# Kernel tuning notes

Measured on AMD Instinct MI355X. Metric: run time of the kernel, lower is better.

Reference implementation:

```python
import jax, jax.numpy as jnp
import numpy as np

N_NODES = 100000
NEG_SLOPE = 0.2


def gat_conv(x, edge_index, W, a_src, a_dst, bias):
    """PyG GATConv, heads=1, concat, add_self_loops=True."""
    N = x.shape[0]
    loop = jnp.arange(N, dtype=edge_index.dtype)
    src = jnp.concatenate([edge_index[0], loop])  # message sources j
    dst = jnp.concatenate([edge_index[1], loop])  # message targets i
    h = x @ W                                      # [N, out]
    asrc = h @ a_src                               # [N]
    adst = h @ a_dst                               # [N]
    e = jax.nn.leaky_relu(asrc[src] + adst[dst], NEG_SLOPE)   # [E+N]
    m = jax.ops.segment_max(e, dst, num_segments=N)           # per-dst max
    w = jnp.exp(e - jax.lax.stop_gradient(m)[dst])
    denom = jax.ops.segment_sum(w, dst, num_segments=N)
    alpha = w / denom[dst]                                     # softmax per dst
    out = jax.ops.segment_sum(alpha[:, None] * h[src], dst, num_segments=N)
    return out + bias


def setup_inputs() -> dict:
    key = jax.random.key(0)
    ks = jax.random.split(key, 16)
    N, E, D = N_NODES, 3200000, 128
    x = jax.random.normal(ks[0], (N, D), dtype=jnp.float32)
    edge_index = jax.random.randint(ks[1], (2, E), 0, N, dtype=jnp.int64)
    def glorot(k, shape):
        fan = sum(shape)
        return jax.random.uniform(k, shape, jnp.float32, -1.0, 1.0) * np.sqrt(6.0 / fan)
    return {
        "x": x,
        "edge_index": edge_index,
        "W1": glorot(ks[2], (D, 16)),
        "a1_src": glorot(ks[3], (16,)),
        "a1_dst": glorot(ks[4], (16,)),
        "b1": jnp.zeros((16,), jnp.float32),
        "W2": glorot(ks[5], (16, 10)),
        "a2_src": glorot(ks[6], (10,)),
        "a2_dst": glorot(ks[7], (10,)),
        "b2": jnp.zeros((10,), jnp.float32),
        "Wl1": glorot(ks[8], (10, 10)),
        "bl1": jnp.zeros((10,), jnp.float32),
        "Wl2": glorot(ks[9], (10, 1)),
        "bl2": jnp.zeros((1,), jnp.float32),
    }


def reference(x, edge_index, W1, a1_src, a1_dst, b1, W2, a2_src, a2_dst, b2,
              Wl1, bl1, Wl2, bl2):
    h = gat_conv(x, edge_index, W1, a1_src, a1_dst, b1)
    h = jax.nn.relu(h)
    h = gat_conv(h, edge_index, W2, a2_src, a2_dst, b2)
    h = h @ Wl1 + bl1
    h = jax.nn.relu(h)
    return h @ Wl2 + bl2  # [N, 1]
```

## Files before the change

### kernel.cpp

```cpp
#include <hip/hip_runtime.h>
#include <hip/hip_fp16.h>


#define NEG 0.2f
#define FSH 7
#define BNODES 128
#define NSBMAX 1024
#define CAPB 4608
#define TILE 4096
#define PES 9

__device__ __forceinline__ float lrelu(float x) { return x > 0.0f ? x : NEG * x; }

__device__ __forceinline__ unsigned fenc(float f) {
    unsigned u = __float_as_uint(f);
    return (u & 0x80000000u) ? ~u : (u | 0x80000000u);
}
__device__ __forceinline__ float fdec(unsigned e) {
    return (e & 0x80000000u) ? __uint_as_float(e & 0x7FFFFFFFu) : __uint_as_float(~e);
}

__device__ __forceinline__ float4 ldh4(const __half* h, size_t off) {
    uint2 u = *(const uint2*)(h + off);
    __half2 a = *(__half2*)&u.x, b = *(__half2*)&u.y;
    float2 fa = __half22float2(a), fb = __half22float2(b);
    return make_float4(fa.x, fa.y, fb.x, fb.y);
}

__global__ __launch_bounds__(256) void k_front(
    const float* __restrict__ x, const float* __restrict__ W1,
    const float* __restrict__ a1s, const float* __restrict__ a1d,
    __half* __restrict__ h1, float* __restrict__ s1, float* __restrict__ d1,
    unsigned* __restrict__ gmax,
    const int* __restrict__ esrc, const int* __restrict__ edst,
    int* __restrict__ bcur, unsigned* __restrict__ pairs,
    int N, int E, int NG, int NC, int NSB)
{
    __shared__ float smem[10500];
    int tid = threadIdx.x;
    int bid = blockIdx.x;
    long long T = (long long)NG + NC;
    int before = (int)(((long long)bid * NC) / T);
    int isc = (int)((((long long)bid + 1) * NC) / T) > before;

    if (isc) {
        unsigned* lsrt = (unsigned*)smem;
        int* lhist = (int*)smem + TILE;
        int* lofs  = lhist + NSBMAX;
        int* gbase = lofs + NSBMAX;
        int* wsum  = gbase + NSBMAX;
        int cid = before;
        int base = cid * TILE;
        int tcnt = min(TILE, E - base);
        for (int i = tid; i < NSB; i += 256) lhist[i] = 0;
        __syncthreads();
        for (int i = tid; i < tcnt; i += 256)
            atomicAdd(&lhist[edst[base + i] >> FSH], 1);
        __syncthreads();
        int i0 = 4 * tid;
        int a0 = (i0 + 0 < NSB) ? lhist[i0 + 0] : 0;
        int a1 = (i0 + 1 < NSB) ? lhist[i0 + 1] : 0;
        int a2 = (i0 + 2 < NSB) ? lhist[i0 + 2] : 0;
        int a3 = (i0 + 3 < NSB) ? lhist[i0 + 3] : 0;
        int s = a0 + a1 + a2 + a3, pfx = s;
#pragma unroll
        for (int off = 1; off < 64; off <<= 1) {
            int t = __shfl_up(pfx, off, 64);
            if ((tid & 63) >= off) pfx += t;
        }
        if ((tid & 63) == 63) wsum[tid >> 6] = pfx;
        __syncthreads();
        int carry = 0;
        for (int w = 0; w < (tid >> 6); ++w) carry += wsum[w];
        int excl = pfx + carry - s;
        if (i0 + 0 < NSB) { lofs[i0 + 0] = excl;                 gbase[i0 + 0] = a0 ? atomicAdd(&bcur[(i0 + 0) * 16], a0) : 0; }
        if (i0 + 1 < NSB) { lofs[i0 + 1] = excl + a0;            gbase[i0 + 1] = a1 ? atomicAdd(&bcur[(i0 + 1) * 16], a1) : 0; }
        if (i0 + 2 < NSB) { lofs[i0 + 2] = excl + a0 + a1;       gbase[i0 + 2] = a2 ? atomicAdd(&bcur[(i0 + 2) * 16], a2) : 0; }
        if (i0 + 3 < NSB) { lofs[i0 + 3] = excl + a0 + a1 + a2;  gbase[i0 + 3] = a3 ? atomicAdd(&bcur[(i0 + 3) * 16], a3) : 0; }
        __syncthreads();
        if (i0 + 0 < NSB) lhist[i0 + 0] = lofs[i0 + 0];
        if (i0 + 1 < NSB) lhist[i0 + 1] = lofs[i0 + 1];
        if (i0 + 2 < NSB) lhist[i0 + 2] = lofs[i0 + 2];
        if (i0 + 3 < NSB) lhist[i0 + 3] = lofs[i0 + 3];
        __syncthreads();
        for (int i = tid; i < tcnt; i += 256) {
            int e = base + i;
            int d = edst[e], srcv = esrc[e];
            int pos = atomicAdd(&lhist[d >> FSH], 1);
            lsrt[pos] = ((unsigned)(d & (BNODES - 1)) << 17) | (unsigned)srcv;
        }
        __syncthreads();
        for (int i = tid; i < tcnt; i += 256) {
            int lo = 0, hi = NSB - 1;
            while (lo < hi) { int mid = (lo + hi + 1) >> 1; if (lofs[mid] <= i) lo = mid; else hi = mid - 1; }
            int rel = gbase[lo] + (i - lofs[lo]);
            if (rel < CAPB) pairs[(size_t)lo * CAPB + rel] = lsrt[i];
        }
        return;
    }

    float* sW = smem;
    float* sx = smem + 2048;
    float* wm = smem + 2048 + 64 * 132;
    int gid = bid - before;
    for (int i = tid; i < 2048; i += 256) sW[i] = W1[i];
    int node0 = gid * 64;
    for (int i = tid; i < 64 * 32; i += 256) {
        int row = i >> 5, c4 = i & 31;
        int n = node0 + row;
        float4 v = make_float4(0.f, 0.f, 0.f, 0.f);
        if (n < N) v = ((const float4*)x)[(size_t)n * 32 + c4];
        *(float4*)&sx[row * 132 + c4 * 4] = v;
    }
    __syncthreads();

    int node = node0 + (tid >> 2);
    int grp  = tid & 3;
    const float* xr = &sx[(tid >> 2) * 132];
    float4 acc = make_float4(0.f, 0.f, 0.f, 0.f);
#pragma unroll 8
    for (int j = 0; j < 128; ++j) {
        float xv = xr[j];
        float4 w = *(const float4*)&sW[j * 16 + grp * 4];
        acc.x += xv * w.x; acc.y += xv * w.y; acc.z += xv * w.z; acc.w += xv * w.w;
    }
    float4 as = ((const float4*)a1s)[grp];
    float4 ad = ((const float4*)a1d)[grp];
    float sv = acc.x * as.x + acc.y * as.y + acc.z * as.z + acc.w * as.w;
    float dv = acc.x * ad.x + acc.y * ad.y + acc.z * ad.z + acc.w * ad.w;
    sv += __shfl_xor(sv, 1); sv += __shfl_xor(sv, 2);
    dv += __shfl_xor(dv, 1); dv += __shfl_xor(dv, 2);
    if (node < N) {
        __half2 p0 = __floats2half2_rn(acc.x, acc.y);
        __half2 p1 = __floats2half2_rn(acc.z, acc.w);
        uint2 u; u.x = *(unsigned*)&p0; u.y = *(unsigned*)&p1;
        *(uint2*)&h1[(size_t)node * 16 + grp * 4] = u;
        if (grp == 0) { s1[node] = sv; d1[node] = dv; }
    }
    float m = (node < N) ? sv : -3.4e38f;
#pragma unroll
    for (int off = 32; off >= 1; off >>= 1) m = fmaxf(m, __shfl_xor(m, off));
    if ((tid & 63) == 0) wm[tid >> 6] = m;
    __syncthreads();
    if (tid == 0) {
        float b = fmaxf(fmaxf(wm[0], wm[1]), fmaxf(wm[2], wm[3]));
        atomicMax(gmax, fenc(b));
    }
}

__global__ __launch_bounds__(512) void k_agg1(
    const int* __restrict__ bcur, const unsigned* __restrict__ pairs,
    const int* __restrict__ esrc, const int* __restrict__ edst,
    const float* __restrict__ s1, const float* __restrict__ d1, const __half* __restrict__ h1,
    const float* __restrict__ b1, const float* __restrict__ W2,
    const float* __restrict__ a2s, const float* __restrict__ a2d,
    __half* __restrict__ h2, float* __restrict__ s2, float* __restrict__ d2,
    const unsigned* __restrict__ gmax1p, unsigned* __restrict__ gmax2, int N, int E)
{
    __shared__ unsigned srt[CAPB];
    __shared__ float accs[BNODES * 17];
    __shared__ int lcnt[BNODES];
    __shared__ int lofs[BNODES + 1];
    __shared__ float dds[BNODES], mbs[BNODES];
    __shared__ float sW[160], sb[16], sas[16], sad[16];
    __shared__ int wsum[8];
    __shared__ float wm[8];

    int tid = threadIdx.x;
    int fb = blockIdx.x;
    if (tid < 160) sW[tid] = W2[tid];
    if (tid < 16) {
        sb[tid]  = b1[tid];
        sas[tid] = (tid < 10) ? a2s[tid] : 0.f;
        sad[tid] = (tid < 10) ? a2d[tid] : 0.f;
    }
    int node0 = fb << FSH;
    float g0 = fdec(*gmax1p);
    if (tid < BNODES) {
        int n = node0 + tid;
        float dd = (n < N) ? d1[n] : 0.f;
        dds[tid] = dd; mbs[tid] = lrelu(g0 + dd);
        lcnt[tid] = 0;
    }
    __syncthreads();

    int rbase = fb * CAPB;
    int cnt = bcur[fb * 16];
    int gg = tid >> 2, q = tid & 3;

    if (cnt <= CAPB) {
        unsigned pe[PES];
#pragma unroll
        for (int u = 0; u < PES; ++u) {
            int i = tid + u * 512;
            bool ok = (i < cnt);
            pe[u] = ok ? pairs[rbase + i] : 0u;
            if (ok) atomicAdd(&lcnt[(pe[u] >> 17) & (BNODES - 1)], 1);
        }
        __syncthreads();
        int c = (tid < BNODES) ? lcnt[tid] : 0;
        int pfx = c;
#pragma unroll
        for (int off = 1; off < 64; off <<= 1) {
            int t = __shfl_up(pfx, off, 64);
            if ((tid & 63) >= off) pfx += t;
        }
        if ((tid & 63) == 63) wsum[tid >> 6] = pfx;
        __syncthreads();
        int carry = 0;
        for (int w = 0; w < (tid >> 6); ++w) carry += wsum[w];
        pfx += carry;
        if (tid < BNODES) { lofs[tid + 1] = pfx; lcnt[tid] = pfx - c; }
        if (tid == 0) lofs[0] = 0;
        __syncthreads();
#pragma unroll
        for (int u = 0; u < PES; ++u) {
            int i = tid + u * 512;
            if (i < cnt) {
                unsigned p = pe[u];
                int pos = atomicAdd(&lcnt[(p >> 17) & (BNODES - 1)], 1);
                srt[pos] = p & 0x1FFFF;
            }
        }
        __syncthreads();

        int n = node0 + gg;
        float4 accv; float den;
        if (n < N) {
            float w = __expf(lrelu(s1[n] + dds[gg]) - mbs[gg]);
            float4 hv = ldh4(h1, (size_t)n * 16 + 4 * q);
            accv = make_float4(w * hv.x, w * hv.y, w * hv.z, w * hv.w);
            den = w;
        } else { accv = make_float4(0.f, 0.f, 0.f, 0.f); den = 0.f; }
        {
            float dd = dds[gg], mb = mbs[gg];
            int j = lofs[gg], j1 = lofs[gg + 1];
            for (; j + 4 <= j1; j += 4) {
                int e0 = srt[j], e1 = srt[j + 1], e2 = srt[j + 2], e3 = srt[j + 3];
                float4 H0 = ldh4(h1, (size_t)e0 * 16 + 4 * q);
                float4 H1 = ldh4(h1, (size_t)e1 * 16 + 4 * q);
                float4 H2 = ldh4(h1, (size_t)e2 * 16 + 4 * q);
                float4 H3 = ldh4(h1, (size_t)e3 * 16 + 4 * q);
                int eq = srt[j + q];
                float wq = __expf(lrelu(s1[eq] + dd) - mb);
                float w0 = __shfl(wq, 0, 4), w1 = __shfl(wq, 1, 4);
                float w2 = __shfl(wq, 2, 4), w3 = __shfl(wq, 3, 4);
                accv.x += w0 * H0.x + w1 * H1.x + w2 * H2.x + w3 * H3.x;
                accv.y += w0 * H0.y + w1 * H1.y + w2 * H2.y + w3 * H3.y;
                accv.z += w0 * H0.z + w1 * H1.z + w2 * H2.z + w3 * H3.z;
                accv.w += w0 * H0.w + w1 * H1.w + w2 * H2.w + w3 * H3.w;
                den += (w0 + w1) + (w2 + w3);
            }
            for (; j < j1; ++j) {
                int e0 = srt[j];
                float w0 = __expf(lrelu(s1[e0] + dd) - mb);
                float4 H0 = ldh4(h1, (size_t)e0 * 16 + 4 * q);
                accv.x += w0 * H0.x; accv.y += w0 * H0.y;
                accv.z += w0 * H0.z; accv.w += w0 * H0.w;
                den += w0;
            }
        }
        accs[gg * 17 + 4 * q + 0] = accv.x;
        accs[gg * 17 + 4 * q + 1] = accv.y;
        accs[gg * 17 + 4 * q + 2] = accv.z;
        accs[gg * 17 + 4 * q + 3] = accv.w;
        if (q == 0) accs[gg * 17 + 16] = den;
        __syncthreads();
    } else {
        for (int i = tid; i < BNODES * 17; i += 512) accs[i] = 0.f;
        __syncthreads();
        if (tid < BNODES) {
            int n = node0 + tid;
            if (n < N) {
                float w = __expf(lrelu(s1[n] + dds[tid]) - mbs[tid]);
#pragma unroll
                for (int t = 0; t < 16; ++t)
                    accs[tid * 17 + t] = w * __half2float(h1[(size_t)n * 16 + t]);
                accs[tid * 17 + 16] = w;
            }
        }
        __syncthreads();
        for (int i = tid; i < E; i += 512) {
            int d = edst[i];
            if ((d >> FSH) != fb) continue;
            int nl = d & (BNODES - 1), src = esrc[i];
            float w = __expf(lrelu(s1[src] + dds[nl]) - mbs[nl]);
#pragma unroll
            for (int t = 0; t < 16; ++t)
                atomicAdd(&accs[nl * 17 + t], w * __half2float(h1[(size_t)src * 16 + t]));
            atomicAdd(&accs[nl * 17 + 16], w);
        }
        __syncthreads();
    }

    int g = tid >> 4, k = tid & 15;
    float sval = -3.4e38f;
#pragma unroll
    for (int qq = 0; qq < 4; ++qq) {
        int nl = g * 4 + qq, nn = node0 + nl;
        if (nn >= N) continue;
        float inv = 1.f / accs[nl * 17 + 16];
        float o = fmaxf(accs[nl * 17 + k] * inv + sb[k], 0.f);
        float hh = 0.f;
#pragma unroll
        for (int kk = 0; kk < 16; ++kk) {
            float ov = __shfl(o, kk, 16);
            if (k < 10) hh += ov * sW[kk * 10 + k];
        }
        if (k >= 10) hh = 0.f;
        float ts = hh * sas[k];
        float td = hh * sad[k];
#pragma unroll
        for (int off = 1; off < 16; off <<= 1) {
            ts += __shfl_xor(ts, off, 16);
            td += __shfl_xor(td, off, 16);
        }
        h2[(size_t)nn * 16 + k] = __float2half_rn(hh);
        if (k == 0) { s2[nn] = ts; d2[nn] = td; }
        sval = fmaxf(sval, ts);
    }
    float m = sval;
#pragma unroll
    for (int off = 32; off >= 1; off >>= 1) m = fmaxf(m, __shfl_xor(m, off));
    if ((tid & 63) == 0) wm[tid >> 6] = m;
    __syncthreads();
    if (tid == 0) {
        float bmx = wm[0];
#pragma unroll
        for (int i = 1; i < 8; ++i) bmx = fmaxf(bmx, wm[i]);
        atomicMax(gmax2, fenc(bmx));
    }
}

__global__ __launch_bounds__(512) void k_agg2(
    const int* __restrict__ bcur, const unsigned* __restrict__ pairs,
    const int* __restrict__ esrc, const int* __restrict__ edst,
    const float* __restrict__ s2, const float* __restrict__ d2, const __half* __restrict__ h2,
    const float* __restrict__ b2, const float* __restrict__ Wl1, const float* __restrict__ bl1,
    const float* __restrict__ Wl2, const float* __restrict__ bl2,
    const unsigned* __restrict__ gmax2p, float* __restrict__ out, int N, int E)
{
    __shared__ unsigned srt[CAPB];
    __shared__ float accs[BNODES * 17];
    __shared__ int lcnt[BNODES];
    __shared__ int lofs[BNODES + 1];
    __shared__ float dds[BNODES], mbs[BNODES];
    __shared__ float sW1[100], sb1[16], sW2[16], sb2g[16];
    __shared__ float sbl2;
    __shared__ int wsum[8];

    int tid = threadIdx.x;
    int fb = blockIdx.x;
    if (tid < 100) sW1[tid] = Wl1[tid];
    if (tid < 16) {
        sb1[tid]  = (tid < 10) ? bl1[tid] : 0.f;
        sW2[tid]  = (tid < 10) ? Wl2[tid] : 0.f;
        sb2g[tid] = (tid < 10) ? b2[tid]  : 0.f;
    }
    if (tid == 0) sbl2 = bl2[0];
    int node0 = fb << FSH;
    float g0 = fdec(*gmax2p);
    if (tid < BNODES) {
        int n = node0 + tid;
        float dd = (n < N) ? d2[n] : 0.f;
        dds[tid] = dd; mbs[tid] = lrelu(g0 + dd);
        lcnt[tid] = 0;
    }
    __syncthreads();

    int rbase = fb * CAPB;
    int cnt = bcur[fb * 16];
    int gg = tid >> 2, q = tid & 3;

    if (cnt <= CAPB) {
        unsigned pe[PES];
#pragma unroll
        for (int u = 0; u < PES; ++u) {
            int i = tid + u * 512;
            bool ok = (i < cnt);
            pe[u] = ok ? pairs[rbase + i] : 0u;
            if (ok) atomicAdd(&lcnt[(pe[u] >> 17) & (BNODES - 1)], 1);
        }
        __syncthreads();
        int c = (tid < BNODES) ? lcnt[tid] : 0;
        int pfx = c;
#pragma unroll
        for (int off = 1; off < 64; off <<= 1) {
            int t = __shfl_up(pfx, off, 64);
            if ((tid & 63) >= off) pfx += t;
        }
        if ((tid & 63) == 63) wsum[tid >> 6] = pfx;
        __syncthreads();
        int carry = 0;
        for (int w = 0; w < (tid >> 6); ++w) carry += wsum[w];
        pfx += carry;
        if (tid < BNODES) { lofs[tid + 1] = pfx; lcnt[tid] = pfx - c; }
        if (tid == 0) lofs[0] = 0;
        __syncthreads();
#pragma unroll
        for (int u = 0; u < PES; ++u) {
            int i = tid + u * 512;
            if (i < cnt) {
                unsigned p = pe[u];
                int pos = atomicAdd(&lcnt[(p >> 17) & (BNODES - 1)], 1);
                srt[pos] = p & 0x1FFFF;
            }
        }
        __syncthreads();

        int n = node0 + gg;
        float4 accv; float den;
        if (n < N) {
            float w = __expf(lrelu(s2[n] + dds[gg]) - mbs[gg]);
            float4 hv = ldh4(h2, (size_t)n * 16 + 4 * q);
            accv = make_float4(w * hv.x, w * hv.y, w * hv.z, w * hv.w);
            den = w;
        } else { accv = make_float4(0.f, 0.f, 0.f, 0.f); den = 0.f; }
        {
            float dd = dds[gg], mb = mbs[gg];
            int j = lofs[gg], j1 = lofs[gg + 1];
            for (; j + 4 <= j1; j += 4) {
                int e0 = srt[j], e1 = srt[j + 1], e2 = srt[j + 2], e3 = srt[j + 3];
                float4 H0 = ldh4(h2, (size_t)e0 * 16 + 4 * q);
                float4 H1 = ldh4(h2, (size_t)e1 * 16 + 4 * q);
                float4 H2 = ldh4(h2, (size_t)e2 * 16 + 4 * q);
                float4 H3 = ldh4(h2, (size_t)e3 * 16 + 4 * q);
                int eq = srt[j + q];
                float wq = __expf(lrelu(s2[eq] + dd) - mb);
                float w0 = __shfl(wq, 0, 4), w1 = __shfl(wq, 1, 4);
                float w2 = __shfl(wq, 2, 4), w3 = __shfl(wq, 3, 4);
                accv.x += w0 * H0.x + w1 * H1.x + w2 * H2.x + w3 * H3.x;
                accv.y += w0 * H0.y + w1 * H1.y + w2 * H2.y + w3 * H3.y;
                accv.z += w0 * H0.z + w1 * H1.z + w2 * H2.z + w3 * H3.z;
                accv.w += w0 * H0.w + w1 * H1.w + w2 * H2.w + w3 * H3.w;
                den += (w0 + w1) + (w2 + w3);
            }
            for (; j < j1; ++j) {
                int e0 = srt[j];
                float w0 = __expf(lrelu(s2[e0] + dd) - mb);
                float4 H0 = ldh4(h2, (size_t)e0 * 16 + 4 * q);
                accv.x += w0 * H0.x; accv.y += w0 * H0.y;
                accv.z += w0 * H0.z; accv.w += w0 * H0.w;
                den += w0;
            }
        }
        accs[gg * 17 + 4 * q + 0] = accv.x;
        accs[gg * 17 + 4 * q + 1] = accv.y;
        accs[gg * 17 + 4 * q + 2] = accv.z;
        accs[gg * 17 + 4 * q + 3] = accv.w;
        if (q == 0) accs[gg * 17 + 16] = den;
        __syncthreads();
    } else {
        for (int i = tid; i < BNODES * 17; i += 512) accs[i] = 0.f;
        __syncthreads();
        if (tid < BNODES) {
            int n = node0 + tid;
            if (n < N) {
                float w = __expf(lrelu(s2[n] + dds[tid]) - mbs[tid]);
#pragma unroll
                for (int t = 0; t < 16; ++t)
                    accs[tid * 17 + t] = w * __half2float(h2[(size_t)n * 16 + t]);
                accs[tid * 17 + 16] = w;
            }
        }
        __syncthreads();
        for (int i = tid; i < E; i += 512) {
            int d = edst[i];
            if ((d >> FSH) != fb) continue;
            int nl = d & (BNODES - 1), src = esrc[i];
            float w = __expf(lrelu(s2[src] + dds[nl]) - mbs[nl]);
#pragma unroll
            for (int t = 0; t < 16; ++t)
                atomicAdd(&accs[nl * 17 + t], w * __half2float(h2[(size_t)src * 16 + t]));
            atomicAdd(&accs[nl * 17 + 16], w);
        }
        __syncthreads();
    }

    int g = tid >> 4, k = tid & 15;
    bool fk = k < 10;
#pragma unroll
    for (int qq = 0; qq < 4; ++qq) {
        int nl = g * 4 + qq, nn = node0 + nl;
        if (nn >= N) continue;
        float inv = 1.f / accs[nl * 17 + 16];
        float o = fk ? accs[nl * 17 + k] * inv + sb2g[k] : 0.f;
        float v = sb1[k];
#pragma unroll
        for (int kk = 0; kk < 10; ++kk) {
            float ov = __shfl(o, kk, 16);
            if (fk) v += ov * sW1[kk * 10 + k];
        }
        float t = fmaxf(v, 0.f);
        float cc = t * sW2[k];
#pragma unroll
        for (int off = 1; off < 16; off <<= 1) cc += __shfl_xor(cc, off, 16);
        if (k == 0) out[nn] = cc + sbl2;
    }
}

extern "C" void kernel_launch(void* const* d_in, const int* in_sizes, int n_in,
                              void* d_out, int out_size, void* d_ws, size_t ws_size,
                              hipStream_t stream)
{
    const float* x   = (const float*)d_in[0];
    const int*   ei  = (const int*)  d_in[1];
    const float* W1  = (const float*)d_in[2];
    const float* a1s = (const float*)d_in[3];
    const float* a1d = (const float*)d_in[4];
    const float* b1  = (const float*)d_in[5];
    const float* W2  = (const float*)d_in[6];
    const float* a2s = (const float*)d_in[7];
    const float* a2d = (const float*)d_in[8];
    const float* b2  = (const float*)d_in[9];
    const float* Wl1 = (const float*)d_in[10];
    const float* bl1 = (const float*)d_in[11];
    const float* Wl2 = (const float*)d_in[12];
    const float* bl2 = (const float*)d_in[13];

    int N = in_sizes[0] / 128;
    int E = in_sizes[1] / 2;
    const int* ei_src = ei;
    const int* ei_dst = ei + E;
    int NSB = (N + BNODES - 1) >> FSH;

    size_t Np = ((size_t)N + 3) & ~(size_t)3;
    size_t need_bytes = (16 + (size_t)NSB * 16) * 4 + Np * 20 * 4 + (size_t)NSB * CAPB * 4;
    if (ws_size < need_bytes) return;

    unsigned* gmax1 = (unsigned*)d_ws;
    unsigned* gmax2 = gmax1 + 1;
    int* bcur = (int*)d_ws + 16;
    float* rest = (float*)d_ws + 16 + (size_t)NSB * 16;
    __half* h1 = (__half*)rest;
    float* s1 = rest + Np * 8;
    float* d1 = s1 + Np;
    __half* h2 = (__half*)(d1 + Np);
    float* s2 = (float*)(h2) + Np * 8;
    float* d2 = s2 + Np;
    unsigned* pairs = (unsigned*)(d2 + Np);

    int NG = (N + 63) / 64;
    int NC = (E + TILE - 1) / TILE;

    hipMemsetAsync(d_ws, 0, (16 + (size_t)NSB * 16) * sizeof(int), stream);
    hipLaunchKernelGGL(k_front, dim3(NG + NC), dim3(256), 0, stream,
                       x, W1, a1s, a1d, h1, s1, d1, gmax1,
                       ei_src, ei_dst, bcur, pairs, N, E, NG, NC, NSB);
    hipLaunchKernelGGL(k_agg1, dim3(NSB), dim3(512), 0, stream,
                       bcur, pairs, ei_src, ei_dst, s1, d1, h1, b1, W2, a2s, a2d,
                       h2, s2, d2, gmax1, gmax2, N, E);
    hipLaunchKernelGGL(k_agg2, dim3(NSB), dim3(512), 0, stream,
                       bcur, pairs, ei_src, ei_dst, s2, d2, h2, b2, Wl1, bl1, Wl2, bl2,
                       gmax2, (float*)d_out, N, E);
}
```

Measured before the change: 279.1 us.

## Reuse agg1 per-bucket sort in agg2 and rework front-kernel scatter and GEMV

k_agg1 writes its locally sorted edge list back into the pairs buffer and stores per-bucket offsets in a new lofs_g array. k_agg2 loads these directly, which removes its histogram, prefix scan and atomic scatter. In k_front, the chunk blocks keep dst values in registers and record a bucket id per sorted slot, replacing the per-element binary search. The GEMV path now reads x straight into registers, splitting K across four lanes and reducing with shuffles instead of staging x in LDS. The cost is extra global writes in agg1 and higher register pressure in the front kernel.

```diff
diff --git a/kernel.cpp b/kernel.cpp
--- a/kernel.cpp
+++ b/kernel.cpp
@@ -8,7 +8,9 @@
 #define NSBMAX 1024
 #define CAPB 4608
 #define TILE 4096
+#define EPT 16
 #define PES 9
+#define LOFSTR 132
 
 __device__ __forceinline__ float lrelu(float x) { return x > 0.0f ? x : NEG * x; }
 
@@ -36,7 +38,7 @@
     int* __restrict__ bcur, unsigned* __restrict__ pairs,
     int N, int E, int NG, int NC, int NSB)
 {
-    __shared__ float smem[10500];
+    __shared__ float smem[9220];
     int tid = threadIdx.x;
     int bid = blockIdx.x;
     long long T = (long long)NG + NC;
@@ -49,13 +51,19 @@
         int* lofs  = lhist + NSBMAX;
         int* gbase = lofs + NSBMAX;
         int* wsum  = gbase + NSBMAX;
+        unsigned short* rid = (unsigned short*)(smem + TILE + 3 * NSBMAX + 4);
         int cid = before;
         int base = cid * TILE;
         int tcnt = min(TILE, E - base);
         for (int i = tid; i < NSB; i += 256) lhist[i] = 0;
         __syncthreads();
-        for (int i = tid; i < tcnt; i += 256)
-            atomicAdd(&lhist[edst[base + i] >> FSH], 1);
+        int ed[EPT];
+#pragma unroll
+        for (int u = 0; u < EPT; ++u) {
+            int i = tid + u * 256;
+            ed[u] = (i < tcnt) ? edst[base + i] : -1;
+            if (ed[u] >= 0) atomicAdd(&lhist[ed[u] >> FSH], 1);
+        }
         __syncthreads();
         int i0 = 4 * tid;
         int a0 = (i0 + 0 < NSB) ? lhist[i0 + 0] : 0;
@@ -83,61 +91,90 @@
         if (i0 + 2 < NSB) lhist[i0 + 2] = lofs[i0 + 2];
         if (i0 + 3 < NSB) lhist[i0 + 3] = lofs[i0 + 3];
         __syncthreads();
+#pragma unroll
+        for (int u = 0; u < EPT; ++u) {
+            int i = tid + u * 256;
+            if (ed[u] >= 0) {
+                int d = ed[u], srcv = esrc[base + i];
+                int b = d >> FSH;
+                int pos = atomicAdd(&lhist[b], 1);
+                lsrt[pos] = ((unsigned)(d & (BNODES - 1)) << 17) | (unsigned)srcv;
+                rid[pos] = (unsigned short)b;
+            }
+        }
+        __syncthreads();
         for (int i = tid; i < tcnt; i += 256) {
-            int e = base + i;
-            int d = edst[e], srcv = esrc[e];
-            int pos = atomicAdd(&lhist[d >> FSH], 1);
-            lsrt[pos] = ((unsigned)(d & (BNODES - 1)) << 17) | (unsigned)srcv;
-        }
-        __syncthreads();
-        for (int i = tid; i < tcnt; i += 256) {
-            int lo = 0, hi = NSB - 1;
-            while (lo < hi) { int mid = (lo + hi + 1) >> 1; if (lofs[mid] <= i) lo = mid; else hi = mid - 1; }
-            int rel = gbase[lo] + (i - lofs[lo]);
-            if (rel < CAPB) pairs[(size_t)lo * CAPB + rel] = lsrt[i];
+            int r = rid[i];
+            int rel = gbase[r] + (i - lofs[r]);
+            if (rel < CAPB) pairs[(size_t)r * CAPB + rel] = lsrt[i];
         }
         return;
     }
 
     float* sW = smem;
-    float* sx = smem + 2048;
-    float* wm = smem + 2048 + 64 * 132;
+    float* wm = smem + 2060;
     int gid = bid - before;
-    for (int i = tid; i < 2048; i += 256) sW[i] = W1[i];
+    for (int i = tid; i < 2048; i += 256) sW[i + ((i >> 9) << 2)] = W1[i];
     int node0 = gid * 64;
-    for (int i = tid; i < 64 * 32; i += 256) {
-        int row = i >> 5, c4 = i & 31;
-        int n = node0 + row;
-        float4 v = make_float4(0.f, 0.f, 0.f, 0.f);
-        if (n < N) v = ((const float4*)x)[(size_t)n * 32 + c4];
-        *(float4*)&sx[row * 132 + c4 * 4] = v;
+    int node = node0 + (tid >> 2);
+    int q = tid & 3;
+    bool valid = node < N;
+    float4 xr[8];
+    {
+        const float4* xp = (const float4*)x + (size_t)node * 32 + q * 8;
+#pragma unroll
+        for (int k = 0; k < 8; ++k)
+            xr[k] = valid ? xp[k] : make_float4(0.f, 0.f, 0.f, 0.f);
     }
     __syncthreads();
 
-    int node = node0 + (tid >> 2);
-    int grp  = tid & 3;
-    const float* xr = &sx[(tid >> 2) * 132];
-    float4 acc = make_float4(0.f, 0.f, 0.f, 0.f);
-#pragma unroll 8
-    for (int j = 0; j < 128; ++j) {
-        float xv = xr[j];
-        float4 w = *(const float4*)&sW[j * 16 + grp * 4];
-        acc.x += xv * w.x; acc.y += xv * w.y; acc.z += xv * w.z; acc.w += xv * w.w;
-    }
-    float4 as = ((const float4*)a1s)[grp];
-    float4 ad = ((const float4*)a1d)[grp];
-    float sv = acc.x * as.x + acc.y * as.y + acc.z * as.z + acc.w * as.w;
-    float dv = acc.x * ad.x + acc.y * ad.y + acc.z * ad.z + acc.w * ad.w;
-    sv += __shfl_xor(sv, 1); sv += __shfl_xor(sv, 2);
-    dv += __shfl_xor(dv, 1); dv += __shfl_xor(dv, 2);
-    if (node < N) {
-        __half2 p0 = __floats2half2_rn(acc.x, acc.y);
-        __half2 p1 = __floats2half2_rn(acc.z, acc.w);
+    float acc[16];
+#pragma unroll
+    for (int c = 0; c < 16; ++c) acc[c] = 0.f;
+    int wbase = q * 516;
+#pragma unroll
+    for (int k = 0; k < 8; ++k) {
+        float xs0 = xr[k].x, xs1 = xr[k].y, xs2 = xr[k].z, xs3 = xr[k].w;
+#pragma unroll
+        for (int t = 0; t < 4; ++t) {
+            float xv = (t == 0) ? xs0 : (t == 1) ? xs1 : (t == 2) ? xs2 : xs3;
+            const float4* wrow = (const float4*)&sW[wbase + (k * 4 + t) * 16];
+            float4 w0 = wrow[0], w1 = wrow[1], w2 = wrow[2], w3 = wrow[3];
+            acc[0]  += xv * w0.x; acc[1]  += xv * w0.y; acc[2]  += xv * w0.z; acc[3]  += xv * w0.w;
+            acc[4]  += xv * w1.x; acc[5]  += xv * w1.y; acc[6]  += xv * w1.z; acc[7]  += xv * w1.w;
+            acc[8]  += xv * w2.x; acc[9]  += xv * w2.y; acc[10] += xv * w2.z; acc[11] += xv * w2.w;
+            acc[12] += xv * w3.x; acc[13] += xv * w3.y; acc[14] += xv * w3.z; acc[15] += xv * w3.w;
+        }
+    }
+#pragma unroll
+    for (int c = 0; c < 16; ++c) {
+        acc[c] += __shfl_xor(acc[c], 1);
+        acc[c] += __shfl_xor(acc[c], 2);
+    }
+    float sv = 0.f, dv = 0.f;
+    {
+        const float4* asp = (const float4*)a1s;
+        const float4* adp = (const float4*)a1d;
+#pragma unroll
+        for (int r = 0; r < 4; ++r) {
+            float4 as = asp[r], ad = adp[r];
+            sv += acc[r*4+0]*as.x + acc[r*4+1]*as.y + acc[r*4+2]*as.z + acc[r*4+3]*as.w;
+            dv += acc[r*4+0]*ad.x + acc[r*4+1]*ad.y + acc[r*4+2]*ad.z + acc[r*4+3]*ad.w;
+        }
+    }
+    if (valid) {
+        float4 av;
+        if      (q == 0) av = make_float4(acc[0],  acc[1],  acc[2],  acc[3]);
+        else if (q == 1) av = make_float4(acc[4],  acc[5],  acc[6],  acc[7]);
+        else if (q == 2) av = make_float4(acc[8],  acc[9],  acc[10], acc[11]);
+        else             av = make_float4(acc[12], acc[13], acc[14], acc[15]);
+        __half2 p0 = __floats2half2_rn(av.x, av.y);
+        __half2 p1 = __floats2half2_rn(av.z, av.w);
         uint2 u; u.x = *(unsigned*)&p0; u.y = *(unsigned*)&p1;
-        *(uint2*)&h1[(size_t)node * 16 + grp * 4] = u;
-        if (grp == 0) { s1[node] = sv; d1[node] = dv; }
-    }
-    float m = (node < N) ? sv : -3.4e38f;
+        *(uint2*)&h1[(size_t)node * 16 + q * 4] = u;
+        if (q == 0) { s1[node] = sv; d1[node] = dv; }
+    }
+    float m = valid ? sv : -3.4e38f;
 #pragma unroll
     for (int off = 32; off >= 1; off >>= 1) m = fmaxf(m, __shfl_xor(m, off));
     if ((tid & 63) == 0) wm[tid >> 6] = m;
@@ -149,13 +186,14 @@
 }
 
 __global__ __launch_bounds__(512) void k_agg1(
-    const int* __restrict__ bcur, const unsigned* __restrict__ pairs,
+    const int* __restrict__ bcur, unsigned* __restrict__ pairs,
     const int* __restrict__ esrc, const int* __restrict__ edst,
     const float* __restrict__ s1, const float* __restrict__ d1, const __half* __restrict__ h1,
     const float* __restrict__ b1, const float* __restrict__ W2,
     const float* __restrict__ a2s, const float* __restrict__ a2d,
     __half* __restrict__ h2, float* __restrict__ s2, float* __restrict__ d2,
-    const unsigned* __restrict__ gmax1p, unsigned* __restrict__ gmax2, int N, int E)
+    const unsigned* __restrict__ gmax1p, unsigned* __restrict__ gmax2,
+    int* __restrict__ lofs_g, int N, int E)
 {
     __shared__ unsigned srt[CAPB];
     __shared__ float accs[BNODES * 17];
@@ -223,6 +261,14 @@
             }
         }
         __syncthreads();
+
+#pragma unroll
+        for (int u = 0; u < PES; ++u) {
+            int i = tid + u * 512;
+            if (i < cnt) pairs[rbase + i] = srt[i];
+        }
+        if (tid <= BNODES) lofs_g[fb * LOFSTR + tid] = lofs[tid];
+        if (tid == 0) lofs_g[fb * LOFSTR + BNODES + 1] = 1;
 
         int n = node0 + gg;
         float4 accv; float den;
@@ -267,6 +313,7 @@
         if (q == 0) accs[gg * 17 + 16] = den;
         __syncthreads();
     } else {
+        if (tid == 0) lofs_g[fb * LOFSTR + BNODES + 1] = 0;
         for (int i = tid; i < BNODES * 17; i += 512) accs[i] = 0.f;
         __syncthreads();
         if (tid < BNODES) {
@@ -333,21 +380,21 @@
 }
 
 __global__ __launch_bounds__(512) void k_agg2(
-    const int* __restrict__ bcur, const unsigned* __restrict__ pairs,
+    const unsigned* __restrict__ pairs,
     const int* __restrict__ esrc, const int* __restrict__ edst,
     const float* __restrict__ s2, const float* __restrict__ d2, const __half* __restrict__ h2,
     const float* __restrict__ b2, const float* __restrict__ Wl1, const float* __restrict__ bl1,
     const float* __restrict__ Wl2, const float* __restrict__ bl2,
-    const unsigned* __restrict__ gmax2p, float* __restrict__ out, int N, int E)
+    const unsigned* __restrict__ gmax2p, const int* __restrict__ lofs_g,
+    float* __restrict__ out, int N, int E)
 {
     __shared__ unsigned srt[CAPB];
     __shared__ float accs[BNODES * 17];
-    __shared__ int lcnt[BNODES];
     __shared__ int lofs[BNODES + 1];
     __shared__ float dds[BNODES], mbs[BNODES];
     __shared__ float sW1[100], sb1[16], sW2[16], sb2g[16];
     __shared__ float sbl2;
-    __shared__ int wsum[8];
+    __shared__ int s_ok;
 
     int tid = threadIdx.x;
     int fb = blockIdx.x;
@@ -358,53 +405,26 @@
         sb2g[tid] = (tid < 10) ? b2[tid]  : 0.f;
     }
     if (tid == 0) sbl2 = bl2[0];
+    if (tid <= BNODES) lofs[tid] = lofs_g[fb * LOFSTR + tid];
+    if (tid == 256) s_ok = lofs_g[fb * LOFSTR + BNODES + 1];
     int node0 = fb << FSH;
     float g0 = fdec(*gmax2p);
     if (tid < BNODES) {
         int n = node0 + tid;
         float dd = (n < N) ? d2[n] : 0.f;
         dds[tid] = dd; mbs[tid] = lrelu(g0 + dd);
-        lcnt[tid] = 0;
     }
     __syncthreads();
 
     int rbase = fb * CAPB;
-    int cnt = bcur[fb * 16];
     int gg = tid >> 2, q = tid & 3;
 
-    if (cnt <= CAPB) {
-        unsigned pe[PES];
+    if (s_ok) {
+        int cnt = lofs[BNODES];
 #pragma unroll
         for (int u = 0; u < PES; ++u) {
             int i = tid + u * 512;
-            bool ok = (i < cnt);
-            pe[u] = ok ? pairs[rbase + i] : 0u;
-            if (ok) atomicAdd(&lcnt[(pe[u] >> 17) & (BNODES - 1)], 1);
-        }
-        __syncthreads();
-        int c = (tid < BNODES) ? lcnt[tid] : 0;
-        int pfx = c;
-#pragma unroll
-        for (int off = 1; off < 64; off <<= 1) {
-            int t = __shfl_up(pfx, off, 64);
-            if ((tid & 63) >= off) pfx += t;
-        }
-        if ((tid & 63) == 63) wsum[tid >> 6] = pfx;
-        __syncthreads();
-        int carry = 0;
-        for (int w = 0; w < (tid >> 6); ++w) carry += wsum[w];
-        pfx += carry;
-        if (tid < BNODES) { lofs[tid + 1] = pfx; lcnt[tid] = pfx - c; }
-        if (tid == 0) lofs[0] = 0;
-        __syncthreads();
-#pragma unroll
-        for (int u = 0; u < PES; ++u) {
-            int i = tid + u * 512;
-            if (i < cnt) {
-                unsigned p = pe[u];
-                int pos = atomicAdd(&lcnt[(p >> 17) & (BNODES - 1)], 1);
-                srt[pos] = p & 0x1FFFF;
-            }
+            if (i < cnt) srt[i] = pairs[rbase + i];
         }
         __syncthreads();
 
@@ -525,7 +545,8 @@
     int NSB = (N + BNODES - 1) >> FSH;
 
     size_t Np = ((size_t)N + 3) & ~(size_t)3;
-    size_t need_bytes = (16 + (size_t)NSB * 16) * 4 + Np * 20 * 4 + (size_t)NSB * CAPB * 4;
+    size_t need_bytes = (16 + (size_t)NSB * 16) * 4 + Np * 20 * 4
+                      + (size_t)NSB * CAPB * 4 + (size_t)NSB * LOFSTR * 4;
     if (ws_size < need_bytes) return;
 
     unsigned* gmax1 = (unsigned*)d_ws;
@@ -539,6 +560,7 @@
     float* s2 = (float*)(h2) + Np * 8;
     float* d2 = s2 + Np;
     unsigned* pairs = (unsigned*)(d2 + Np);
+    int* lofs_g = (int*)(pairs + (size_t)NSB * CAPB);
 
     int NG = (N + 63) / 64;
     int NC = (E + TILE - 1) / TILE;
@@ -549,8 +571,8 @@
                        ei_src, ei_dst, bcur, pairs, N, E, NG, NC, NSB);
     hipLaunchKernelGGL(k_agg1, dim3(NSB), dim3(512), 0, stream,
                        bcur, pairs, ei_src, ei_dst, s1, d1, h1, b1, W2, a2s, a2d,
-                       h2, s2, d2, gmax1, gmax2, N, E);
+                       h2, s2, d2, gmax1, gmax2, lofs_g, N, E);
     hipLaunchKernelGGL(k_agg2, dim3(NSB), dim3(512), 0, stream,
-                       bcur, pairs, ei_src, ei_dst, s2, d2, h2, b2, Wl1, bl1, Wl2, bl2,
-                       gmax2, (float*)d_out, N, E);
-}
+                       pairs, ei_src, ei_dst, s2, d2, h2, b2, Wl1, bl1, Wl2, bl2,
+                       gmax2, lofs_g, (float*)d_out, N, E);
+}
```

Result: faster. 263.5 us (-5.6%).
